# Kernel optimization log

Hardware: AMD Instinct MI355X
Metric: run time of the kernel (lower is better)

The kernel has to match this reference:

```python
import jax, jax.numpy as jnp
import numpy as np

SPU_ZERO = float(np.sqrt(0.5))  # sqrt(|spu(0)|), spu(0) = -0.5


def spu(x):
    # spu(x) = x^2 - 0.5 for x >= 0, sigmoid(-x) - 1 for x < 0
    return jnp.where(x >= 0, x * x - 0.5, jax.nn.sigmoid(-x) - 1.0)


def dspu(x):
    s = jax.nn.sigmoid(-x)
    return jnp.where(x >= 0, 2.0 * x, -s * (1.0 - s))


def setup_inputs() -> dict:
    key = jax.random.key(0)
    k1, k2, k3 = jax.random.split(key, 3)
    N = 16777216
    lower = jax.random.normal(k1, (N,), dtype=jnp.float32)
    width = jnp.abs(jax.random.normal(k2, (N,), dtype=jnp.float32)) + 1e-3
    upper = lower + width
    t = jax.random.uniform(k3, (N,), dtype=jnp.float32)
    x = lower + t * width  # concrete point inside the interval
    return {"x": x, "lower_bounds": lower, "upper_bounds": upper}


def reference(x, lower_bounds, upper_bounds):
    l = lower_bounds
    u = upper_bounds
    sl = spu(l)
    su = spu(u)
    slope = (su - sl) / (u - l)  # chord slope
    chord_b = sl - slope * l

    # case 2 (l >= 0) tangent at midpoint
    a2 = (u + l) * 0.5
    wl2 = dspu(a2)
    bl2 = spu(a2) - a2 * wl2

    # case 3 (l < 0 <= u, u >= spu_zero) tangent at max(mid, spu_zero)
    a3 = jnp.maximum(a2, SPU_ZERO)
    wl3 = dspu(a3)
    bl3 = spu(a3) - a3 * wl3

    # case 4 (l < 0, 0 < u < spu_zero)
    flat4 = sl > su
    wu4 = jnp.where(flat4, 0.0, slope)
    bu4 = jnp.where(flat4, jnp.maximum(sl, su), chord_b)

    c1 = u <= 0
    c2 = l >= 0
    c3 = u >= SPU_ZERO

    w_u = jnp.where(c1, 0.0,
          jnp.where(c2, u + l,
          jnp.where(c3, slope, wu4)))
    b_u = jnp.where(c1, sl,
          jnp.where(c2, -u * l + 0.5,  # -u*l - spu(0)
          jnp.where(c3, chord_b, bu4)))
    w_l = jnp.where(c1, slope,
          jnp.where(c2, wl2,
          jnp.where(c3, wl3, 0.0)))
    b_l = jnp.where(c1, chord_b,
          jnp.where(c2, bl2,
          jnp.where(c3, bl3, -0.5)))  # spu(0) = -0.5

    out = spu(x)
    # weights are eye with modified diagonal -> diagonal matmul is elementwise
    new_lower = w_l * l + b_l
    new_upper = w_u * u + b_u
    return (out, new_lower, new_upper)
```

## Files before the change

### kernel.cpp

```cpp
#include <hip/hip_runtime.h>
#include <math.h>

#define SPU_ZERO 0.70710678118654752440f

__device__ __forceinline__ float spu_f(float x) {
    if (x >= 0.0f) return x * x - 0.5f;
    float s = 1.0f / (1.0f + expf(x));
    return s - 1.0f;
}

__device__ __forceinline__ float dspu_f(float x) {
    if (x >= 0.0f) return 2.0f * x;
    float s = 1.0f / (1.0f + expf(x));
    return -s * (1.0f - s);
}

__device__ __forceinline__ void spu_transform(float x, float l, float u,
                                              float& o, float& nl, float& nu) {
    float sl = spu_f(l);
    float su = spu_f(u);
    float slope = (su - sl) / (u - l);
    float chord_b = sl - slope * l;

    float w_u, b_u, w_l, b_l;
    if (u <= 0.0f) {
        w_u = 0.0f;   b_u = sl;
        w_l = slope;  b_l = chord_b;
    } else if (l >= 0.0f) {
        float a2 = 0.5f * (u + l);
        float wl2 = 2.0f * a2;
        float bl2 = (a2 * a2 - 0.5f) - a2 * wl2;
        w_u = u + l;  b_u = 0.5f - u * l;
        w_l = wl2;    b_l = bl2;
    } else if (u >= SPU_ZERO) {
        float a2 = 0.5f * (u + l);
        float a3 = fmaxf(a2, SPU_ZERO);
        float wl3 = 2.0f * a3;
        float bl3 = (a3 * a3 - 0.5f) - a3 * wl3;
        w_u = slope;  b_u = chord_b;
        w_l = wl3;    b_l = bl3;
    } else {
        bool flat4 = sl > su;
        w_u = flat4 ? 0.0f : slope;
        b_u = flat4 ? fmaxf(sl, su) : chord_b;
        w_l = 0.0f;   b_l = -0.5f;
    }

    o  = spu_f(x);
    nl = w_l * l + b_l;
    nu = w_u * u + b_u;
}

__global__ void __launch_bounds__(256)
spu_kernel_v4(const float4* __restrict__ xs,
              const float4* __restrict__ ls,
              const float4* __restrict__ us,
              float4* __restrict__ out, int n4) {
    int i = blockIdx.x * blockDim.x + threadIdx.x;
    if (i >= n4) return;

    float4 xv = xs[i];
    float4 lv = ls[i];
    float4 uv = us[i];
    float4 o, nl, nu;

    spu_transform(xv.x, lv.x, uv.x, o.x, nl.x, nu.x);
    spu_transform(xv.y, lv.y, uv.y, o.y, nl.y, nu.y);
    spu_transform(xv.z, lv.z, uv.z, o.z, nl.z, nu.z);
    spu_transform(xv.w, lv.w, uv.w, o.w, nl.w, nu.w);

    out[i]           = o;
    out[n4 + i]      = nl;
    out[2 * n4 + i]  = nu;
}

__global__ void __launch_bounds__(64)
spu_kernel_tail(const float* __restrict__ xs,
                const float* __restrict__ ls,
                const float* __restrict__ us,
                float* __restrict__ out, int n, int start) {
    int i = start + blockIdx.x * blockDim.x + threadIdx.x;
    if (i >= n) return;
    float o, nl, nu;
    spu_transform(xs[i], ls[i], us[i], o, nl, nu);
    out[i]         = o;
    out[n + i]     = nl;
    out[2 * n + i] = nu;
}

extern "C" void kernel_launch(void* const* d_in, const int* in_sizes, int n_in,
                              void* d_out, int out_size, void* d_ws, size_t ws_size,
                              hipStream_t stream) {
    const float* x = (const float*)d_in[0];
    const float* l = (const float*)d_in[1];
    const float* u = (const float*)d_in[2];
    float* out = (float*)d_out;
    int n = in_sizes[0];
    int n4 = n / 4;
    int rem = n - n4 * 4;

    if (n4 > 0) {
        int blocks = (n4 + 255) / 256;
        spu_kernel_v4<<<blocks, 256, 0, stream>>>(
            (const float4*)x, (const float4*)l, (const float4*)u,
            (float4*)out, n4);
    }
    if (rem > 0) {
        spu_kernel_tail<<<1, 64, 0, stream>>>(x, l, u, out, n, n4 * 4);
    }
}
```

Before: 338.0 us.

## Process two float4 chunks per thread with nontemporal loads/stores and branchless SPU

```diff
diff --git a/kernel.cpp b/kernel.cpp
--- a/kernel.cpp
+++ b/kernel.cpp
@@ -3,75 +3,89 @@
 
 #define SPU_ZERO 0.70710678118654752440f
 
-__device__ __forceinline__ float spu_f(float x) {
-    if (x >= 0.0f) return x * x - 0.5f;
-    float s = 1.0f / (1.0f + expf(x));
-    return s - 1.0f;
-}
+typedef float f4 __attribute__((ext_vector_type(4)));
 
-__device__ __forceinline__ float dspu_f(float x) {
-    if (x >= 0.0f) return 2.0f * x;
-    float s = 1.0f / (1.0f + expf(x));
-    return -s * (1.0f - s);
+__device__ __forceinline__ float spu_b(float v) {
+    float e   = expf(v);
+    float s   = 1.0f / (1.0f + e);
+    float neg = s - 1.0f;
+    float pos = fmaf(v, v, -0.5f);
+    return v >= 0.0f ? pos : neg;
 }
 
 __device__ __forceinline__ void spu_transform(float x, float l, float u,
                                               float& o, float& nl, float& nu) {
-    float sl = spu_f(l);
-    float su = spu_f(u);
-    float slope = (su - sl) / (u - l);
-    float chord_b = sl - slope * l;
+    float sl = spu_b(l);
+    float su = spu_b(u);
+    float slope   = (su - sl) / (u - l);
+    float chord_b = fmaf(-slope, l, sl);
 
-    float w_u, b_u, w_l, b_l;
-    if (u <= 0.0f) {
-        w_u = 0.0f;   b_u = sl;
-        w_l = slope;  b_l = chord_b;
-    } else if (l >= 0.0f) {
-        float a2 = 0.5f * (u + l);
-        float wl2 = 2.0f * a2;
-        float bl2 = (a2 * a2 - 0.5f) - a2 * wl2;
-        w_u = u + l;  b_u = 0.5f - u * l;
-        w_l = wl2;    b_l = bl2;
-    } else if (u >= SPU_ZERO) {
-        float a2 = 0.5f * (u + l);
-        float a3 = fmaxf(a2, SPU_ZERO);
-        float wl3 = 2.0f * a3;
-        float bl3 = (a3 * a3 - 0.5f) - a3 * wl3;
-        w_u = slope;  b_u = chord_b;
-        w_l = wl3;    b_l = bl3;
-    } else {
-        bool flat4 = sl > su;
-        w_u = flat4 ? 0.0f : slope;
-        b_u = flat4 ? fmaxf(sl, su) : chord_b;
-        w_l = 0.0f;   b_l = -0.5f;
+    bool c1 = u <= 0.0f;
+    bool c2 = l >= 0.0f;
+    bool c3 = u >= SPU_ZERO;
+
+    float a2 = 0.5f * (u + l);
+    float at = c2 ? a2 : fmaxf(a2, SPU_ZERO);
+    float wt = at + at;
+    float bt = fmaf(-at, at, -0.5f);
+
+    bool  flat4 = sl > su;
+    float wu4 = flat4 ? 0.0f : slope;
+    float bu4 = flat4 ? sl   : chord_b;
+
+    bool tang = c2 || c3;
+    float w_u = c1 ? 0.0f    : (c2 ? (u + l)            : (c3 ? slope   : wu4));
+    float b_u = c1 ? sl      : (c2 ? fmaf(-u, l, 0.5f)  : (c3 ? chord_b : bu4));
+    float w_l = c1 ? slope   : (tang ? wt : 0.0f);
+    float b_l = c1 ? chord_b : (tang ? bt : -0.5f);
+
+    o  = spu_b(x);
+    nl = fmaf(w_l, l, b_l);
+    nu = fmaf(w_u, u, b_u);
+}
+
+__device__ __forceinline__ void spu_transform4(f4 xv, f4 lv, f4 uv,
+                                               f4& ov, f4& nlv, f4& nuv) {
+#pragma unroll
+    for (int k = 0; k < 4; ++k) {
+        float o, nl, nu;
+        spu_transform(xv[k], lv[k], uv[k], o, nl, nu);
+        ov[k] = o; nlv[k] = nl; nuv[k] = nu;
     }
-
-    o  = spu_f(x);
-    nl = w_l * l + b_l;
-    nu = w_u * u + b_u;
 }
 
 __global__ void __launch_bounds__(256)
-spu_kernel_v4(const float4* __restrict__ xs,
-              const float4* __restrict__ ls,
-              const float4* __restrict__ us,
-              float4* __restrict__ out, int n4) {
-    int i = blockIdx.x * blockDim.x + threadIdx.x;
+spu_kernel_v5(const f4* __restrict__ xs,
+              const f4* __restrict__ ls,
+              const f4* __restrict__ us,
+              f4* __restrict__ out, int n4) {
+    const int T = gridDim.x * blockDim.x;
+    const int i = blockIdx.x * blockDim.x + threadIdx.x;
     if (i >= n4) return;
 
-    float4 xv = xs[i];
-    float4 lv = ls[i];
-    float4 uv = us[i];
-    float4 o, nl, nu;
+    const int  j  = i + T;
+    const bool bj = j < n4;
+    const int  jc = bj ? j : i;
 
-    spu_transform(xv.x, lv.x, uv.x, o.x, nl.x, nu.x);
-    spu_transform(xv.y, lv.y, uv.y, o.y, nl.y, nu.y);
-    spu_transform(xv.z, lv.z, uv.z, o.z, nl.z, nu.z);
-    spu_transform(xv.w, lv.w, uv.w, o.w, nl.w, nu.w);
+    f4 x0 = __builtin_nontemporal_load(xs + i);
+    f4 l0 = __builtin_nontemporal_load(ls + i);
+    f4 u0 = __builtin_nontemporal_load(us + i);
+    f4 x1 = __builtin_nontemporal_load(xs + jc);
+    f4 l1 = __builtin_nontemporal_load(ls + jc);
+    f4 u1 = __builtin_nontemporal_load(us + jc);
 
-    out[i]           = o;
-    out[n4 + i]      = nl;
-    out[2 * n4 + i]  = nu;
+    f4 o0, nl0, nu0, o1, nl1, nu1;
+    spu_transform4(x0, l0, u0, o0, nl0, nu0);
+    spu_transform4(x1, l1, u1, o1, nl1, nu1);
+
+    __builtin_nontemporal_store(o0,  out + i);
+    __builtin_nontemporal_store(nl0, out + n4 + i);
+    __builtin_nontemporal_store(nu0, out + 2 * n4 + i);
+    if (bj) {
+        __builtin_nontemporal_store(o1,  out + j);
+        __builtin_nontemporal_store(nl1, out + n4 + j);
+        __builtin_nontemporal_store(nu1, out + 2 * n4 + j);
+    }
 }
 
 __global__ void __launch_bounds__(64)
@@ -95,15 +109,14 @@
     const float* l = (const float*)d_in[1];
     const float* u = (const float*)d_in[2];
     float* out = (float*)d_out;
-    int n = in_sizes[0];
+    int n  = in_sizes[0];
     int n4 = n / 4;
     int rem = n - n4 * 4;
 
     if (n4 > 0) {
-        int blocks = (n4 + 255) / 256;
-        spu_kernel_v4<<<blocks, 256, 0, stream>>>(
-            (const float4*)x, (const float4*)l, (const float4*)u,
-            (float4*)out, n4);
+        int blocks = (n4 + 2 * 256 - 1) / (2 * 256);
+        spu_kernel_v5<<<blocks, 256, 0, stream>>>(
+            (const f4*)x, (const f4*)l, (const f4*)u, (f4*)out, n4);
     }
     if (rem > 0) {
         spu_kernel_tail<<<1, 64, 0, stream>>>(x, l, u, out, n, n4 * 4);
```

Result: faster. 326.0 us (-3.6%).
